# Kernel tuning notes

Hardware: AMD Instinct MI355X
Metric: run time of the kernel (lower is better)

## Reference

```python
import jax, jax.numpy as jnp
import numpy as np

TOPK = 8
N_EXPERTS = 64
ROUTE_SCALE = 1.0


def setup_inputs() -> dict:
    key = jax.random.key(0)
    k1, k2 = jax.random.split(key)
    x = jax.random.normal(k1, (16, 256, 64, 64), dtype=jnp.float32)
    gate_w = jax.random.normal(k2, (64, 256, 3, 3), dtype=jnp.float32) * 0.02  # [E, C, kh, kw]
    bias = jnp.zeros((64,), dtype=jnp.float32)  # load-balancing bias buffer
    return {"x": x, "gate_w": gate_w, "bias": bias}


def reference(x, gate_w, bias):
    # 3x3 conv, stride 1, pad 1 (SAME), no conv bias -> expert logits [B, E, H, W]
    logits = jax.lax.conv_general_dilated(
        x, gate_w, window_strides=(1, 1), padding="SAME",
        dimension_numbers=("NCHW", "OIHW", "NCHW"))
    scores = jax.nn.sigmoid(logits)                 # [B, E, H, W]
    s = jnp.moveaxis(scores, 1, -1)                 # [B, H, W, E]
    biased = s + bias                               # bias broadcast over experts
    _, idx = jax.lax.top_k(biased, TOPK)            # [B, H, W, K] (topk on biased scores)
    w = jnp.take_along_axis(s, idx, axis=-1)        # gather UNbiased scores
    w = jax.nn.softmax(w, axis=-1) * ROUTE_SCALE    # softmax over the K selected experts
    weights = jnp.moveaxis(w, -1, 1)                # [B, K, H, W] to match torch layout
    indices = jnp.moveaxis(idx, -1, 1)              # [B, K, H, W]
    counts = jnp.zeros((N_EXPERTS,), jnp.int32).at[idx.ravel()].add(1)  # bincount
    return weights, indices, counts
```

## Files before the change

### kernel.cpp

```cpp
#include <hip/hip_runtime.h>


typedef _Float16 half8 __attribute__((ext_vector_type(8)));
typedef __attribute__((ext_vector_type(4))) float f32x4;

#define LOG2E 1.44269504f

__device__ __forceinline__ unsigned short f2h_bits(float f) {
    _Float16 h = (_Float16)f;
    unsigned short b;
    __builtin_memcpy(&b, &h, 2);
    return b;
}

constexpr int WB_U4 = 8 * 9 * 4 * 64;
constexpr size_t XT_BYTES = (size_t)16 * 66 * 8 * 66 * 32 * 2;
constexpr size_t WS_NEED  = XT_BYTES + (size_t)WB_U4 * 16 + 262144;

#define GLOAD16(gp, lp)                                                    \
    __builtin_amdgcn_global_load_lds(                                      \
        (const __attribute__((address_space(1))) void*)(gp),               \
        (__attribute__((address_space(3))) void*)(lp), 16, 0, 0)


constexpr int NB_INT = 2048, NB_BOR = 130, NB_WB = 72;
constexpr int PREP_GRID = NB_INT + NB_BOR + NB_WB;

__global__ __launch_bounds__(256) void prep_all3(
    const float* __restrict__ x, const float* __restrict__ gw,
    _Float16* __restrict__ xT, unsigned short* __restrict__ wB,
    float* __restrict__ out) {
    const int blk = blockIdx.x, tid = threadIdx.x;
    if (blk < NB_INT) {
        int gid = blk * 256 + tid;
        int w = gid & 63, q = (gid >> 6) & 7, h = (gid >> 9) & 63, b = gid >> 15;
        const float* src = x + (((b * 256 + q * 32) * 64 + h) * 64 + w);
        float v[32];
#pragma unroll
        for (int j = 0; j < 32; ++j) v[j] = src[j * 4096];
        uint4 pk[4];
#pragma unroll
        for (int c8 = 0; c8 < 4; ++c8) {
            pk[c8].x = (unsigned)f2h_bits(v[c8 * 8 + 0]) | ((unsigned)f2h_bits(v[c8 * 8 + 1]) << 16);
            pk[c8].y = (unsigned)f2h_bits(v[c8 * 8 + 2]) | ((unsigned)f2h_bits(v[c8 * 8 + 3]) << 16);
            pk[c8].z = (unsigned)f2h_bits(v[c8 * 8 + 4]) | ((unsigned)f2h_bits(v[c8 * 8 + 5]) << 16);
            pk[c8].w = (unsigned)f2h_bits(v[c8 * 8 + 6]) | ((unsigned)f2h_bits(v[c8 * 8 + 7]) << 16);
        }
        size_t site = ((size_t)(b * 66 + h + 1) * 8 + q) * 66 + (w + 1);
        uint4* dst = (uint4*)xT + site * 4;
        dst[0] = pk[0]; dst[1] = pk[1]; dst[2] = pk[2]; dst[3] = pk[3];
    } else if (blk < NB_INT + NB_BOR) {
        int t = (blk - NB_INT) * 256 + tid;
        int q = t & 7, site = t >> 3;
        int sb = site / 260, s = site - sb * 260;
        int hp, wp;
        if (s < 132) { hp = (s >= 66) ? 65 : 0; wp = (s >= 66) ? (s - 66) : s; }
        else         { int s2 = s - 132; hp = 1 + (s2 >> 1); wp = (s2 & 1) * 65; }
        uint4 z = {0u, 0u, 0u, 0u};
        size_t idx = ((((size_t)sb * 66 + hp) * 8 + q) * 66 + wp) * 32;
        uint4* dst = (uint4*)(xT + idx);
#pragma unroll
        for (int k = 0; k < 4; ++k) dst[k] = z;
    } else {
        int wblk = blk - (NB_INT + NB_BOR);
        if (wblk == 0 && tid < 64) out[1048576 + tid] = 0.f;
        int g = wblk * 256 + tid;
        int lane = g & 63;
        int nt   = (g >> 6) & 3;
        int rest = g >> 8;
        int t = rest % 9, q = rest / 9;
        int e  = nt * 16 + (lane & 15);
        int c0 = q * 32 + (lane >> 4) * 8;
        unsigned short o[8];
#pragma unroll
        for (int j = 0; j < 8; ++j)
            o[j] = f2h_bits(gw[(e * 256 + c0 + j) * 9 + t]);
        uint4 pk;
        pk.x = (unsigned)o[0] | ((unsigned)o[1] << 16);
        pk.y = (unsigned)o[2] | ((unsigned)o[3] << 16);
        pk.z = (unsigned)o[4] | ((unsigned)o[5] << 16);
        pk.w = (unsigned)o[6] | ((unsigned)o[7] << 16);
        ((uint4*)wB)[g] = pk;
    }
}

constexpr int SSTR = 68;
constexpr int HALFB = 12672;

__global__ __launch_bounds__(256, 4) void gate_main4(
    const _Float16* __restrict__ xT, const float* __restrict__ bias,
    const unsigned short* __restrict__ wB, float* __restrict__ out) {
    __shared__ uint4 smem4[2 * HALFB / 16];
    __shared__ float bias_s[64];
    __shared__ int   hist[64];
    char* smem = (char*)smem4;

    const int tid  = threadIdx.x;
    const int lane = tid & 63;
    const int rw   = tid >> 6;
    const int blk  = blockIdx.x;
    const int b    = blk & 15;
    const int r    = blk >> 4;

    if (tid < 64) { bias_s[tid] = bias[tid]; hist[tid] = 0; }

    const int ph = rw >> 1, eh = rw & 1;

    const _Float16* srcP[4];
    int ldsOff[4];
    const bool act3 = (tid < 24);
#pragma unroll
    for (int i = 0; i < 4; ++i) {
        int T = tid + i * 256;
        if (T >= 792) T = 0;
        int seg = T / 264, o = T - seg * 264;
        int osrc = (o & ~3) | ((o & 3) ^ ((o >> 3) & 3));
        srcP[i]  = xT + ((size_t)(b * 66 + r + seg) * 8) * 2112 + osrc * 8;
        ldsOff[i] = T * 16;
    }
    auto STAGE = [&](int q, int halfB) {
#pragma unroll
        for (int i = 0; i < 3; ++i)
            GLOAD16(srcP[i] + q * 2112, smem + ldsOff[i] + halfB);
        if (act3)
            GLOAD16(srcP[3] + q * 2112, smem + ldsOff[3] + halfB);
    };

    const int wl = ph * 32 + (lane & 15);
    const char* aB[3];
#pragma unroll
    for (int kw = 0; kw < 3; ++kw) {
        int wp = wl + kw;
        int c8 = (lane >> 4) ^ ((wp >> 1) & 3);
        aB[kw] = smem + wp * 64 + c8 * 16;
    }

    half8 Aa[3][2];
    uint4 Bb[6][2];
    f32x4 acc[2][2];
#pragma unroll
    for (int mt = 0; mt < 2; ++mt)
#pragma unroll
        for (int nt = 0; nt < 2; ++nt) acc[mt][nt] = (f32x4){0.f, 0.f, 0.f, 0.f};

    auto LDA = [&](int kh, int kw, int slot, int HB) {
        Aa[slot][0] = *(const half8*)(aB[kw] + HB + kh * 4224);
        Aa[slot][1] = *(const half8*)(aB[kw] + HB + kh * 4224 + 1024);
    };
    const char* bP = (const char*)wB + eh * 2048 + lane * 16;
    auto LDB = [&](int slot) {
        Bb[slot][0] = *(const uint4*)bP;
        Bb[slot][1] = *(const uint4*)(bP + 1024);
        bP += 4096;
    };
    auto MT = [&](int as, int bs) {
#pragma unroll
        for (int nt = 0; nt < 2; ++nt) {
            half8 bfr;
            __builtin_memcpy(&bfr, &Bb[bs][nt], 16);
#pragma unroll
            for (int m = 0; m < 2; ++m)
                acc[m][nt] = __builtin_amdgcn_mfma_f32_16x16x32_f16(
                    Aa[as][m], bfr, acc[m][nt], 0, 0, 0);
        }
    };
    auto SB = []() { __builtin_amdgcn_sched_barrier(0); };

    STAGE(0, 0);
    LDB(0); LDB(1); LDB(2); LDB(3); LDB(4); LDB(5);
    SB();
    asm volatile("s_waitcnt vmcnt(12)" ::: "memory");
    __builtin_amdgcn_s_barrier();
    SB();

#pragma unroll 1
    for (int i = 0; i < 4; ++i) {
        STAGE(2 * i + 1, HALFB);
        LDA(0, 0, 0, 0); LDA(0, 1, 1, 0); LDA(0, 2, 2, 0);
        SB();
        MT(0, 0); LDA(1, 0, 0, 0); LDB(0); SB();
        MT(1, 1); LDA(1, 1, 1, 0); LDB(1); SB();
        MT(2, 2); LDA(1, 2, 2, 0); LDB(2); SB();
        MT(0, 3); LDA(2, 0, 0, 0); LDB(3); SB();
        MT(1, 4); LDA(2, 1, 1, 0); LDB(4); SB();
        MT(2, 5); LDA(2, 2, 2, 0); LDB(5); SB();
        MT(0, 0); LDB(0); SB();
        MT(1, 1); LDB(1); SB();
        MT(2, 2); LDB(2); SB();
        SB();
        asm volatile("s_waitcnt vmcnt(18) lgkmcnt(0)" ::: "memory");
        __builtin_amdgcn_s_barrier();
        SB();
        if (i < 3) STAGE(2 * i + 2, 0);
        LDA(0, 0, 0, HALFB); LDA(0, 1, 1, HALFB); LDA(0, 2, 2, HALFB);
        SB();
        MT(0, 3); LDA(1, 0, 0, HALFB); LDB(3); SB();
        MT(1, 4); LDA(1, 1, 1, HALFB); LDB(4); SB();
        MT(2, 5); LDA(1, 2, 2, HALFB); LDB(5); SB();
        MT(0, 0); LDA(2, 0, 0, HALFB); LDB(0); SB();
        MT(1, 1); LDA(2, 1, 1, HALFB); LDB(1); SB();
        MT(2, 2); LDA(2, 2, 2, HALFB); LDB(2); SB();
        MT(0, 3); LDB(3); SB();
        MT(1, 4); LDB(4); SB();
        MT(2, 5); LDB(5); SB();
        if (i < 3) {
            SB();
            asm volatile("s_waitcnt vmcnt(18) lgkmcnt(0)" ::: "memory");
            __builtin_amdgcn_s_barrier();
            SB();
        }
    }
    __syncthreads();

    float* scf = (float*)smem4;
#pragma unroll
    for (int mt = 0; mt < 2; ++mt)
#pragma unroll
        for (int nt = 0; nt < 2; ++nt)
#pragma unroll
            for (int rr = 0; rr < 4; ++rr) {
                float v = acc[mt][nt][rr];
                float s = 1.f / (1.f + __builtin_amdgcn_exp2f(-v * LOG2E));
                int p = ph * 32 + mt * 16 + ((lane >> 4) << 2) + rr;
                int e = eh * 32 + nt * 16 + (lane & 15);
                scf[p * SSTR + e] = s;
            }
    __syncthreads();

    if (tid < 64) {
        const float* row = scf + tid * SSTR;
        float tv[8];
        int   ti[8];
#pragma unroll
        for (int k = 0; k < 8; ++k) { tv[k] = -3.0e38f; ti[k] = 0; }
#pragma unroll
        for (int j4 = 0; j4 < 16; ++j4) {
            f32x4 blkv = *(const f32x4*)(row + j4 * 4);
#pragma unroll
            for (int j = 0; j < 4; ++j) {
                int   e  = j4 * 4 + j;
                float bs = blkv[j] + bias_s[e];
                if (bs > tv[7]) {
                    tv[7] = bs; ti[7] = e;
#pragma unroll
                    for (int k = 7; k > 0; --k) {
                        float fa = tv[k - 1], fb = tv[k];
                        int   ia = ti[k - 1], ib = ti[k];
                        bool  sw = fb > fa;
                        tv[k - 1] = sw ? fb : fa; tv[k] = sw ? fa : fb;
                        ti[k - 1] = sw ? ib : ia; ti[k] = sw ? ia : ib;
                    }
                }
            }
        }
        float u[8], mx = -3.0e38f;
#pragma unroll
        for (int k = 0; k < 8; ++k) { u[k] = tv[k] - bias_s[ti[k]]; mx = fmaxf(mx, u[k]); }
        float ex[8], sum = 0.f;
#pragma unroll
        for (int k = 0; k < 8; ++k) { ex[k] = __builtin_amdgcn_exp2f((u[k] - mx) * LOG2E); sum += ex[k]; }
        float inv = 1.f / sum;

        int obase = b * 32768 + r * 64 + tid;
#pragma unroll
        for (int k = 0; k < 8; ++k) {
            out[obase + k * 4096]          = ex[k] * inv;
            out[524288 + obase + k * 4096] = (float)ti[k];
            atomicAdd(&hist[ti[k]], 1);
        }
    }
    __syncthreads();
    if (tid < 64) atomicAdd(out + 1048576 + tid, (float)hist[tid]);
}


__global__ __launch_bounds__(256) void gate_prep(const float* __restrict__ gw,
                                                 unsigned short* __restrict__ wB,
                                                 float* __restrict__ out) {
    int g = blockIdx.x * 256 + threadIdx.x;
    if (blockIdx.x == 0 && threadIdx.x < 64) out[1048576 + threadIdx.x] = 0.f;
    if (g >= WB_U4) return;
    int lane = g & 63;
    int nt   = (g >> 6) & 3;
    int rest = g >> 8;
    int t = rest % 9, q = rest / 9;
    int e  = nt * 16 + (lane & 15);
    int c0 = q * 32 + (lane >> 4) * 8;
    unsigned short o[8];
#pragma unroll
    for (int j = 0; j < 8; ++j)
        o[j] = f2h_bits(gw[(e * 256 + c0 + j) * 9 + t]);
    uint4 pk;
    pk.x = (unsigned)o[0] | ((unsigned)o[1] << 16);
    pk.y = (unsigned)o[2] | ((unsigned)o[3] << 16);
    pk.z = (unsigned)o[4] | ((unsigned)o[5] << 16);
    pk.w = (unsigned)o[6] | ((unsigned)o[7] << 16);
    ((uint4*)wB)[g] = pk;
}

constexpr int CSTR = 40;
constexpr int SLAB = 3 * 66 * CSTR;

__global__ __launch_bounds__(256, 4) void gate_main_fb(
    const float* __restrict__ x, const float* __restrict__ bias,
    const unsigned short* __restrict__ wB, float* __restrict__ out) {
    __shared__ unsigned short xs[2 * SLAB];
    __shared__ float bias_s[64];
    __shared__ int   hist[64];

    const int tid  = threadIdx.x;
    const int lane = tid & 63;
    const int rw   = tid >> 6;
    const int blk  = blockIdx.x;
    const int b    = blk & 15;
    const int r    = blk >> 4;

    if (tid < 64) { bias_s[tid] = bias[tid]; hist[tid] = 0; }
    {
        uint4 z = {0u, 0u, 0u, 0u};
        uint4* p = (uint4*)xs;
#pragma unroll
        for (int i = 0; i < 8; ++i) {
            int idx = tid + i * 256;
            if (idx < 2 * SLAB / 8) p[idx] = z;
        }
    }

    bool tOk[4];
    int  tSrc[4], tDst[4];
#pragma unroll
    for (int i = 0; i < 4; ++i) {
        int T = tid + i * 256;
        bool ex = (T < 792);
        int chh = T / 198, s = T - chh * 198;
        int row2 = s / 66, wp = s - row2 * 66;
        int gr = r - 1 + row2, gwc = wp - 1;
        tOk[i]  = ex && (gr >= 0) && (gr < 64) && (gwc >= 0) && (gwc < 64);
        tSrc[i] = ((b * 256 + chh * 8) * 64 + gr) * 64 + gwc;
        tDst[i] = (row2 * 66 + wp) * CSTR + chh * 8;
    }

    float tb[4][8];
    auto issueT = [&](int i, int dq) {
        if (tOk[i]) {
            const float* p = x + tSrc[i] + dq * 131072;
#pragma unroll
            for (int u = 0; u < 8; ++u) tb[i][u] = p[u * 4096];
        }
    };
    auto commitT = [&](int i, unsigned short* dst) {
        if (tOk[i]) {
            uint4 pk;
            pk.x = (unsigned)f2h_bits(tb[i][0]) | ((unsigned)f2h_bits(tb[i][1]) << 16);
            pk.y = (unsigned)f2h_bits(tb[i][2]) | ((unsigned)f2h_bits(tb[i][3]) << 16);
            pk.z = (unsigned)f2h_bits(tb[i][4]) | ((unsigned)f2h_bits(tb[i][5]) << 16);
            pk.w = (unsigned)f2h_bits(tb[i][6]) | ((unsigned)f2h_bits(tb[i][7]) << 16);
            *(uint4*)(dst + tDst[i]) = pk;
        }
    };

    const int ph = rw >> 1, eh = rw & 1;
    half8 Aa[3][2];
    uint4 Bb[3][2];
    auto prefA = [&](const unsigned short* buf, int t, int slot) {
        const int kh = t / 3, kw = t % 3;
        const unsigned short* abase =
            buf + (kh * 66 + ph * 32 + (lane & 15) + kw) * CSTR + (lane >> 4) * 8;
#pragma unroll
        for (int mt = 0; mt < 2; ++mt)
            Aa[slot][mt] = *(const half8*)(abase + mt * 16 * CSTR);
    };
    auto prefB = [&](int T9, int slot) {
        const uint4* bp = (const uint4*)wB + (T9 * 4 + eh * 2) * 64 + lane;
#pragma unroll
        for (int nt = 0; nt < 2; ++nt) Bb[slot][nt] = bp[nt * 64];
    };

    f32x4 acc[2][2];
#pragma unroll
    for (int mt = 0; mt < 2; ++mt)
#pragma unroll
        for (int nt = 0; nt < 2; ++nt) acc[mt][nt] = (f32x4){0.f, 0.f, 0.f, 0.f};

    auto mfma_tap = [&](int slot) {
#pragma unroll
        for (int nt = 0; nt < 2; ++nt) {
            half8 bfr;
            __builtin_memcpy(&bfr, &Bb[slot][nt], 16);
#pragma unroll
            for (int mt = 0; mt < 2; ++mt)
                acc[mt][nt] = __builtin_amdgcn_mfma_f32_16x16x32_f16(
                    Aa[slot][mt], bfr, acc[mt][nt], 0, 0, 0);
        }
    };

    __syncthreads();
    issueT(0, 0); issueT(1, 0); issueT(2, 0); issueT(3, 0);
    commitT(0, xs); commitT(1, xs); commitT(2, xs); commitT(3, xs);
    issueT(0, 1); issueT(1, 1); issueT(2, 1); issueT(3, 1);
    prefB(0, 0); prefB(1, 1); prefB(2, 2);
    __syncthreads();

#pragma unroll 1
    for (int q = 0; q < 8; ++q) {
        const unsigned short* cur = xs + (q & 1) * SLAB;
        unsigned short*       nxt = xs + ((q + 1) & 1) * SLAB;
        const int  T0  = q * 9;
        const bool cmt = (q < 7);
        const bool iss = (q < 6);

        prefA(cur, 0, 0); prefA(cur, 1, 1);
        mfma_tap(0); prefB(T0 + 3, 0); prefA(cur, 2, 2);
        mfma_tap(1); prefB(T0 + 4, 1); prefA(cur, 3, 0);
        if (cmt) { commitT(0, nxt); commitT(1, nxt); }
        mfma_tap(2); prefB(T0 + 5, 2); prefA(cur, 4, 1);
        mfma_tap(0); prefB(T0 + 6, 0); prefA(cur, 5, 2);
        if (cmt) { commitT(2, nxt); commitT(3, nxt); }
        mfma_tap(1); prefB(T0 + 7, 1); prefA(cur, 6, 0);
        mfma_tap(2); prefB(T0 + 8, 2); prefA(cur, 7, 1);
        __builtin_amdgcn_sched_barrier(0);
        if (iss) { issueT(0, q + 2); issueT(1, q + 2); issueT(2, q + 2); issueT(3, q + 2); }
        __builtin_amdgcn_sched_barrier(0);
        mfma_tap(0); if (cmt) prefB(T0 + 9, 0);  prefA(cur, 8, 2);
        mfma_tap(1); if (cmt) prefB(T0 + 10, 1);
        mfma_tap(2); if (cmt) prefB(T0 + 11, 2);
        __syncthreads();
    }

    float* scf2 = (float*)xs;
#pragma unroll
    for (int mt = 0; mt < 2; ++mt)
#pragma unroll
        for (int nt = 0; nt < 2; ++nt)
#pragma unroll
            for (int rr = 0; rr < 4; ++rr) {
                float v = acc[mt][nt][rr];
                float s = 1.f / (1.f + __builtin_amdgcn_exp2f(-v * LOG2E));
                int p = ph * 32 + mt * 16 + ((lane >> 4) << 2) + rr;
                int e = eh * 32 + nt * 16 + (lane & 15);
                scf2[p * SSTR + e] = s;
            }
    __syncthreads();

    if (tid < 64) {
        const float* row = scf2 + tid * SSTR;
        float tv[8];
        int   ti[8];
#pragma unroll
        for (int k = 0; k < 8; ++k) { tv[k] = -3.0e38f; ti[k] = 0; }
#pragma unroll
        for (int j4 = 0; j4 < 16; ++j4) {
            f32x4 blkv = *(const f32x4*)(row + j4 * 4);
#pragma unroll
            for (int j = 0; j < 4; ++j) {
                int   e  = j4 * 4 + j;
                float bs = blkv[j] + bias_s[e];
                if (bs > tv[7]) {
                    tv[7] = bs; ti[7] = e;
#pragma unroll
                    for (int k = 7; k > 0; --k) {
                        float fa = tv[k - 1], fb = tv[k];
                        int   ia = ti[k - 1], ib = ti[k];
                        bool  sw = fb > fa;
                        tv[k - 1] = sw ? fb : fa; tv[k] = sw ? fa : fb;
                        ti[k - 1] = sw ? ib : ia; ti[k] = sw ? ia : ib;
                    }
                }
            }
        }
        float u[8], mx = -3.0e38f;
#pragma unroll
        for (int k = 0; k < 8; ++k) { u[k] = tv[k] - bias_s[ti[k]]; mx = fmaxf(mx, u[k]); }
        float ex[8], sum = 0.f;
#pragma unroll
        for (int k = 0; k < 8; ++k) { ex[k] = __builtin_amdgcn_exp2f((u[k] - mx) * LOG2E); sum += ex[k]; }
        float inv = 1.f / sum;

        int obase = b * 32768 + r * 64 + tid;
#pragma unroll
        for (int k = 0; k < 8; ++k) {
            out[obase + k * 4096]          = ex[k] * inv;
            out[524288 + obase + k * 4096] = (float)ti[k];
            atomicAdd(&hist[ti[k]], 1);
        }
    }
    __syncthreads();
    if (tid < 64) atomicAdd(out + 1048576 + tid, (float)hist[tid]);
}

extern "C" void kernel_launch(void* const* d_in, const int* in_sizes, int n_in,
                              void* d_out, int out_size, void* d_ws, size_t ws_size,
                              hipStream_t stream) {
    const float* x    = (const float*)d_in[0];
    const float* gw   = (const float*)d_in[1];
    const float* bias = (const float*)d_in[2];
    float* out = (float*)d_out;

    if (ws_size >= WS_NEED) {
        _Float16* xT = (_Float16*)d_ws;
        unsigned short* wB = (unsigned short*)((char*)d_ws + XT_BYTES);
        prep_all3<<<PREP_GRID, 256, 0, stream>>>(x, gw, xT, wB, out);
        gate_main4<<<1024, 256, 0, stream>>>(xT, bias, wB, out);
    } else {
        unsigned short* wB = (unsigned short*)d_ws;
        gate_prep<<<72, 256, 0, stream>>>(gw, wB, out);
        gate_main_fb<<<1024, 256, 0, stream>>>(x, bias, wB, out);
    }
}
```

Baseline: 158.8 us.

## Give each wave private LDS staging to drop block barriers in conv pipeline

Each wave now stages its own copy of the input rows it needs into a private LDS slice, so the main loop needs only per-wave vmcnt waits instead of block-wide s_barrier syncs. The prologue issues two stages ahead and the loop is re-scheduled with A loads interleaved across the buffer switch. Wave pairs that share a pixel half now load overlapping data redundantly. LDS use roughly doubles and launch bounds drop to 3 blocks per CU, which may reduce occupancy.

```diff
diff --git a/kernel.cpp b/kernel.cpp
--- a/kernel.cpp
+++ b/kernel.cpp
@@ -85,12 +85,13 @@
 }
 
 constexpr int SSTR = 68;
-constexpr int HALFB = 12672;
-
-__global__ __launch_bounds__(256, 4) void gate_main4(
+constexpr int WSL  = 13056;
+constexpr int HB1  = 6528;
+
+__global__ __launch_bounds__(256, 3) void gate_main5(
     const _Float16* __restrict__ xT, const float* __restrict__ bias,
     const unsigned short* __restrict__ wB, float* __restrict__ out) {
-    __shared__ uint4 smem4[2 * HALFB / 16];
+    __shared__ uint4 smem4[4 * WSL / 16];
     __shared__ float bias_s[64];
     __shared__ int   hist[64];
     char* smem = (char*)smem4;
@@ -105,34 +106,34 @@
     if (tid < 64) { bias_s[tid] = bias[tid]; hist[tid] = 0; }
 
     const int ph = rw >> 1, eh = rw & 1;
-
-    const _Float16* srcP[4];
-    int ldsOff[4];
-    const bool act3 = (tid < 24);
-#pragma unroll
-    for (int i = 0; i < 4; ++i) {
-        int T = tid + i * 256;
-        if (T >= 792) T = 0;
-        int seg = T / 264, o = T - seg * 264;
-        int osrc = (o & ~3) | ((o & 3) ^ ((o >> 3) & 3));
-        srcP[i]  = xT + ((size_t)(b * 66 + r + seg) * 8) * 2112 + osrc * 8;
-        ldsOff[i] = T * 16;
-    }
-    auto STAGE = [&](int q, int halfB) {
-#pragma unroll
-        for (int i = 0; i < 3; ++i)
-            GLOAD16(srcP[i] + q * 2112, smem + ldsOff[i] + halfB);
-        if (act3)
-            GLOAD16(srcP[3] + q * 2112, smem + ldsOff[3] + halfB);
-    };
-
-    const int wl = ph * 32 + (lane & 15);
+    char* wbase = smem + rw * WSL;
+
+    const _Float16* srcB[7];
+    int loff[7];
+#pragma unroll
+    for (int i = 0; i < 7; ++i) {
+        int g = lane + i * 64;
+        if (g >= 408) g = 0;
+        int st = g >> 2, c8s = g & 3;
+        int seg = st / 34, s = st - seg * 34;
+        int c8 = c8s ^ ((s >> 1) & 3);
+        srcB[i] = xT + ((size_t)((b * 66 + r + seg) * 8)) * 2112
+                     + (ph * 32 + s) * 32 + c8 * 8;
+        loff[i] = rw * WSL + g * 16;
+    }
+    const bool act6 = (lane < 24);
+    auto STAGE = [&](int q, int HB) {
+#pragma unroll
+        for (int i = 0; i < 6; ++i) GLOAD16(srcB[i] + q * 2112, smem + loff[i] + HB);
+        if (act6) GLOAD16(srcB[6] + q * 2112, smem + loff[6] + HB);
+    };
+
     const char* aB[3];
 #pragma unroll
     for (int kw = 0; kw < 3; ++kw) {
-        int wp = wl + kw;
-        int c8 = (lane >> 4) ^ ((wp >> 1) & 3);
-        aB[kw] = smem + wp * 64 + c8 * 16;
+        int s  = (lane & 15) + kw;
+        int c8 = (lane >> 4) ^ ((s >> 1) & 3);
+        aB[kw] = wbase + s * 64 + c8 * 16;
     }
 
     half8 Aa[3][2];
@@ -144,8 +145,8 @@
         for (int nt = 0; nt < 2; ++nt) acc[mt][nt] = (f32x4){0.f, 0.f, 0.f, 0.f};
 
     auto LDA = [&](int kh, int kw, int slot, int HB) {
-        Aa[slot][0] = *(const half8*)(aB[kw] + HB + kh * 4224);
-        Aa[slot][1] = *(const half8*)(aB[kw] + HB + kh * 4224 + 1024);
+        Aa[slot][0] = *(const half8*)(aB[kw] + HB + kh * 2176);
+        Aa[slot][1] = *(const half8*)(aB[kw] + HB + kh * 2176 + 1024);
     };
     const char* bP = (const char*)wB + eh * 2048 + lane * 16;
     auto LDB = [&](int slot) {
@@ -164,51 +165,42 @@
                     Aa[as][m], bfr, acc[m][nt], 0, 0, 0);
         }
     };
-    auto SB = []() { __builtin_amdgcn_sched_barrier(0); };
+    auto SB  = []() { __builtin_amdgcn_sched_barrier(0); };
+    auto VM18 = []() { asm volatile("s_waitcnt vmcnt(18)" ::: "memory"); };
 
     STAGE(0, 0);
-    LDB(0); LDB(1); LDB(2); LDB(3); LDB(4); LDB(5);
+    LDB(0); LDB(1); LDB(2);
+    STAGE(1, HB1);
+    LDB(3); LDB(4); LDB(5);
     SB();
-    asm volatile("s_waitcnt vmcnt(12)" ::: "memory");
-    __builtin_amdgcn_s_barrier();
+    asm volatile("s_waitcnt vmcnt(19)" ::: "memory");
+    LDA(0, 0, 0, 0); LDA(0, 1, 1, 0); LDA(0, 2, 2, 0);
     SB();
 
 #pragma unroll 1
     for (int i = 0; i < 4; ++i) {
-        STAGE(2 * i + 1, HALFB);
-        LDA(0, 0, 0, 0); LDA(0, 1, 1, 0); LDA(0, 2, 2, 0);
-        SB();
         MT(0, 0); LDA(1, 0, 0, 0); LDB(0); SB();
         MT(1, 1); LDA(1, 1, 1, 0); LDB(1); SB();
         MT(2, 2); LDA(1, 2, 2, 0); LDB(2); SB();
         MT(0, 3); LDA(2, 0, 0, 0); LDB(3); SB();
         MT(1, 4); LDA(2, 1, 1, 0); LDB(4); SB();
         MT(2, 5); LDA(2, 2, 2, 0); LDB(5); SB();
-        MT(0, 0); LDB(0); SB();
-        MT(1, 1); LDB(1); SB();
-        MT(2, 2); LDB(2); SB();
-        SB();
-        asm volatile("s_waitcnt vmcnt(18) lgkmcnt(0)" ::: "memory");
-        __builtin_amdgcn_s_barrier();
-        SB();
+        MT(0, 0); VM18(); LDA(0, 0, 0, HB1);
         if (i < 3) STAGE(2 * i + 2, 0);
-        LDA(0, 0, 0, HALFB); LDA(0, 1, 1, HALFB); LDA(0, 2, 2, HALFB);
-        SB();
-        MT(0, 3); LDA(1, 0, 0, HALFB); LDB(3); SB();
-        MT(1, 4); LDA(1, 1, 1, HALFB); LDB(4); SB();
-        MT(2, 5); LDA(1, 2, 2, HALFB); LDB(5); SB();
-        MT(0, 0); LDA(2, 0, 0, HALFB); LDB(0); SB();
-        MT(1, 1); LDA(2, 1, 1, HALFB); LDB(1); SB();
-        MT(2, 2); LDA(2, 2, 2, HALFB); LDB(2); SB();
-        MT(0, 3); LDB(3); SB();
-        MT(1, 4); LDB(4); SB();
-        MT(2, 5); LDB(5); SB();
-        if (i < 3) {
-            SB();
-            asm volatile("s_waitcnt vmcnt(18) lgkmcnt(0)" ::: "memory");
-            __builtin_amdgcn_s_barrier();
-            SB();
-        }
+        LDB(0); SB();
+        MT(1, 1); LDA(0, 1, 1, HB1); LDB(1); SB();
+        MT(2, 2); LDA(0, 2, 2, HB1); LDB(2); SB();
+        MT(0, 3); LDA(1, 0, 0, HB1); LDB(3); SB();
+        MT(1, 4); LDA(1, 1, 1, HB1); LDB(4); SB();
+        MT(2, 5); LDA(1, 2, 2, HB1); LDB(5); SB();
+        MT(0, 0); LDA(2, 0, 0, HB1); LDB(0); SB();
+        MT(1, 1); LDA(2, 1, 1, HB1); LDB(1); SB();
+        MT(2, 2); LDA(2, 2, 2, HB1); LDB(2); SB();
+        MT(0, 3); VM18(); LDA(0, 0, 0, 0);
+        if (i < 3) STAGE(2 * i + 3, HB1);
+        LDB(3); SB();
+        MT(1, 4); LDA(0, 1, 1, 0); LDB(4); SB();
+        MT(2, 5); LDA(0, 2, 2, 0); LDB(5); SB();
     }
     __syncthreads();
 
@@ -500,7 +492,7 @@
         _Float16* xT = (_Float16*)d_ws;
         unsigned short* wB = (unsigned short*)((char*)d_ws + XT_BYTES);
         prep_all3<<<PREP_GRID, 256, 0, stream>>>(x, gw, xT, wB, out);
-        gate_main4<<<1024, 256, 0, stream>>>(xT, bias, wB, out);
+        gate_main5<<<1024, 256, 0, stream>>>(xT, bias, wB, out);
     } else {
         unsigned short* wB = (unsigned short*)d_ws;
         gate_prep<<<72, 256, 0, stream>>>(gw, wB, out);
```

Result: slower. 165.0 us (+3.9%).
